# Kernel optimization log

Measured on AMD Instinct MI355X. Metric: run time of the kernel, lower is better.

## Reference

```python
import jax, jax.numpy as jnp
import numpy as np

STRIDES = [8, 16, 32, 64, 128]
CELL_ANCHORS = np.array([
 [[-18.0,-8.0,25.0,15.0],[-23.7183,-11.1191,30.7183,18.1191],[-30.9228,-15.0488,37.9228,22.0488],[-12.0,-12.0,19.0,19.0],[-16.1587,-16.1587,23.1587,23.1587],[-21.3984,-21.3984,28.3984,28.3984],[-8.0,-20.0,15.0,27.0],[-11.1191,-26.2381,18.1191,33.2381],[-15.0488,-34.0976,22.0488,41.0976]],
 [[-38.0,-16.0,53.0,31.0],[-49.9564,-22.2381,64.9564,37.2381],[-65.0204,-30.0976,80.0204,45.0976],[-24.0,-24.0,39.0,39.0],[-32.3175,-32.3175,47.3175,47.3175],[-42.7968,-42.7968,57.7968,57.7968],[-14.0,-36.0,29.0,51.0],[-19.7183,-47.4365,34.7183,62.4365],[-26.9228,-61.8456,41.9228,76.8456]],
 [[-74.0,-28.0,105.0,59.0],[-97.3929,-39.4365,128.3929,70.4365],[-126.8661,-53.8456,157.8661,84.8456],[-48.0,-48.0,79.0,79.0],[-64.6349,-64.6349,95.6349,95.6349],[-85.5937,-85.5937,116.5937,116.5937],[-30.0,-76.0,61.0,107.0],[-41.9564,-99.9127,72.9564,130.9127],[-57.0204,-130.0409,88.0204,161.0409]],
 [[-150.0,-60.0,213.0,123.0],[-197.3056,-83.9127,260.3056,146.9127],[-256.907,-114.0409,319.907,177.0409],[-96.0,-96.0,159.0,159.0],[-129.2699,-129.2699,192.2699,192.2699],[-171.1873,-171.1873,234.1873,234.1873],[-58.0,-148.0,121.0,211.0],[-81.3929,-194.7858,144.3929,257.7858],[-110.8661,-253.7322,173.8661,316.7322]],
 [[-298.0,-116.0,425.0,243.0],[-392.0914,-162.7858,519.0914,289.7858],[-510.6392,-221.7322,637.6392,348.7322],[-192.0,-192.0,319.0,319.0],[-258.5398,-258.5398,385.5398,385.5398],[-342.3747,-342.3747,469.3747,469.3747],[-118.0,-300.0,245.0,427.0],[-165.3056,-394.6113,292.3056,521.6113],[-224.907,-513.814,351.907,640.814]]], dtype=np.float32)
THRESHOLD = 0.05
TOP_N = 1000
NMS_THR = 0.5
DETECTIONS = 100


def conv3x3(x, w, b):
    y = jax.lax.conv_general_dilated(x, w, (1, 1), ((1, 1), (1, 1)),
                                     dimension_numbers=('NCHW', 'OIHW', 'NCHW'))
    return y + b[None, :, None, None]


def run_head(x, ws, bs):
    for w, b in zip(ws[:-1], bs[:-1]):
        x = jax.nn.relu(conv3x3(x, w, b))
    return conv3x3(x, ws[-1], bs[-1])


def delta2box(deltas, anchors, w, h, stride):
    awh = anchors[:, 2:] - anchors[:, :2] + 1.0
    ctr = anchors[:, :2] + 0.5 * awh
    pctr = deltas[:, :2] * awh + ctr
    pwh = jnp.exp(deltas[:, 2:]) * awh
    M = jnp.array([w * stride - 1.0, h * stride - 1.0], dtype=deltas.dtype)
    clamp = lambda t: jnp.clip(t, 0.0, M)
    return jnp.concatenate([clamp(pctr - 0.5 * pwh), clamp(pctr + 0.5 * pwh - 1.0)], axis=1)


def decode_level(cls_map, box_map, stride, anchors):
    # cls_map: (B, A*C, H, W) post-sigmoid; box_map: (B, A*4, H, W)
    B, AC, H, W = cls_map.shape
    A = anchors.shape[0]
    C = AC // A

    def one(cm, bm):
        flat = cm.reshape(-1)                      # (A*C*H*W,)
        scores, idx = jax.lax.top_k(flat, TOP_N)
        cls = (idx // (W * H)) % C
        x = idx % W
        y = (idx // W) % H
        a = idx // (C * H * W)
        deltas = bm.reshape(A, 4, H, W)[a, :, y, x]      # (TOP_N, 4)
        grid = jnp.stack([x, y, x, y], axis=1).astype(flat.dtype) * stride + anchors[a]
        boxes = delta2box(deltas, grid, W, H, stride)
        valid = scores >= THRESHOLD                # emulates threshold filter + zero padding
        return (jnp.where(valid, scores, 0.0),
                jnp.where(valid[:, None], boxes, 0.0),
                jnp.where(valid, cls.astype(flat.dtype), 0.0))

    return jax.vmap(one)(cls_map, box_map)


def nms_all(scores, boxes, classes):
    # per-class greedy NMS, fixed DETECTIONS output slots
    def one(s, b, c):
        order = jnp.argsort(-s)
        s, b, c = s[order], b[order], c[order]
        areas = (b[:, 2] - b[:, 0] + 1.0) * (b[:, 3] - b[:, 1] + 1.0)
        state = (s > 0,
                 jnp.zeros((DETECTIONS,), s.dtype),
                 jnp.zeros((DETECTIONS, 4), s.dtype),
                 jnp.zeros((DETECTIONS,), s.dtype))

        def body(i, st):
            valid, os_, ob_, oc_ = st
            any_v = jnp.any(valid)
            idx = jnp.argmax(valid)                # first remaining box (highest score)
            bi, si, ci, ai = b[idx], s[idx], c[idx], areas[idx]
            xy1 = jnp.maximum(b[:, :2], bi[:2])
            xy2 = jnp.minimum(b[:, 2:], bi[2:])
            inter = jnp.prod(jnp.clip(xy2 - xy1 + 1.0, 0.0, None), axis=1)
            iou = inter / (areas + ai - inter)
            suppress = (s <= si) & (iou > NMS_THR) & (c == ci)
            valid = valid & jnp.where(any_v, ~suppress, True)
            os_ = os_.at[i].set(jnp.where(any_v, si, 0.0))
            ob_ = ob_.at[i].set(jnp.where(any_v, bi, jnp.zeros_like(bi)))
            oc_ = oc_.at[i].set(jnp.where(any_v, ci, 0.0))
            return (valid, os_, ob_, oc_)

        _, os_, ob_, oc_ = jax.lax.fori_loop(0, DETECTIONS, body, state)
        return os_, ob_, oc_

    return jax.vmap(one)(scores, boxes, classes)


def _forward(feats, cls_ws, cls_bs, box_ws, box_bs):
    cls_heads = [jax.nn.sigmoid(run_head(f, cls_ws, cls_bs)) for f in feats]
    box_heads = [run_head(f, box_ws, box_bs) for f in feats]
    parts = [decode_level(ch, bh, STRIDES[i], jnp.asarray(CELL_ANCHORS[i]))
             for i, (ch, bh) in enumerate(zip(cls_heads, box_heads))]
    scores = jnp.concatenate([p[0] for p in parts], axis=1)
    boxes = jnp.concatenate([p[1] for p in parts], axis=1)
    classes = jnp.concatenate([p[2] for p in parts], axis=1)
    return nms_all(scores, boxes, classes)


def setup_inputs() -> dict:
    key = jax.random.key(0)
    ks = jax.random.split(key, 32)
    B = 2
    sizes = [64, 32, 16, 8, 4]
    inp = {}
    for i, s in enumerate(sizes):
        inp['feat%d' % i] = jax.random.normal(ks[i], (B, 256, s, s), jnp.float32)
    cls_out = [256, 256, 256, 256, 720]
    box_out = [256, 256, 256, 256, 36]
    for i in range(5):
        inp['cls_w%d' % i] = jax.random.normal(ks[5 + i], (cls_out[i], 256, 3, 3), jnp.float32) * 0.01
        inp['cls_b%d' % i] = jnp.zeros((cls_out[i],), jnp.float32)
        inp['box_w%d' % i] = jax.random.normal(ks[15 + i], (box_out[i], 256, 3, 3), jnp.float32) * 0.01
        inp['box_b%d' % i] = jnp.zeros((box_out[i],), jnp.float32)
    return inp


def reference(feat0, feat1, feat2, feat3, feat4,
              cls_w0, cls_w1, cls_w2, cls_w3, cls_w4,
              cls_b0, cls_b1, cls_b2, cls_b3, cls_b4,
              box_w0, box_w1, box_w2, box_w3, box_w4,
              box_b0, box_b1, box_b2, box_b3, box_b4):
    feats = [feat0, feat1, feat2, feat3, feat4]
    cls_ws = [cls_w0, cls_w1, cls_w2, cls_w3, cls_w4]
    cls_bs = [cls_b0, cls_b1, cls_b2, cls_b3, cls_b4]
    box_ws = [box_w0, box_w1, box_w2, box_w3, box_w4]
    box_bs = [box_b0, box_b1, box_b2, box_b3, box_b4]
    return _forward(feats, cls_ws, cls_bs, box_ws, box_bs)
```

## Files before the change

### kernel.cpp

```cpp
#include <hip/hip_runtime.h>
#include <math.h>

typedef unsigned long long U64;
#define CCAP 4096

__constant__ float cANCH[180] = {
  -18.0f,-8.0f,25.0f,15.0f, -23.7183f,-11.1191f,30.7183f,18.1191f, -30.9228f,-15.0488f,37.9228f,22.0488f,
  -12.0f,-12.0f,19.0f,19.0f, -16.1587f,-16.1587f,23.1587f,23.1587f, -21.3984f,-21.3984f,28.3984f,28.3984f,
  -8.0f,-20.0f,15.0f,27.0f, -11.1191f,-26.2381f,18.1191f,33.2381f, -15.0488f,-34.0976f,22.0488f,41.0976f,
  -38.0f,-16.0f,53.0f,31.0f, -49.9564f,-22.2381f,64.9564f,37.2381f, -65.0204f,-30.0976f,80.0204f,45.0976f,
  -24.0f,-24.0f,39.0f,39.0f, -32.3175f,-32.3175f,47.3175f,47.3175f, -42.7968f,-42.7968f,57.7968f,57.7968f,
  -14.0f,-36.0f,29.0f,51.0f, -19.7183f,-47.4365f,34.7183f,62.4365f, -26.9228f,-61.8456f,41.9228f,76.8456f,
  -74.0f,-28.0f,105.0f,59.0f, -97.3929f,-39.4365f,128.3929f,70.4365f, -126.8661f,-53.8456f,157.8661f,84.8456f,
  -48.0f,-48.0f,79.0f,79.0f, -64.6349f,-64.6349f,95.6349f,95.6349f, -85.5937f,-85.5937f,116.5937f,116.5937f,
  -30.0f,-76.0f,61.0f,107.0f, -41.9564f,-99.9127f,72.9564f,130.9127f, -57.0204f,-130.0409f,88.0204f,161.0409f,
  -150.0f,-60.0f,213.0f,123.0f, -197.3056f,-83.9127f,260.3056f,146.9127f, -256.907f,-114.0409f,319.907f,177.0409f,
  -96.0f,-96.0f,159.0f,159.0f, -129.2699f,-129.2699f,192.2699f,192.2699f, -171.1873f,-171.1873f,234.1873f,234.1873f,
  -58.0f,-148.0f,121.0f,211.0f, -81.3929f,-194.7858f,144.3929f,257.7858f, -110.8661f,-253.7322f,173.8661f,316.7322f,
  -298.0f,-116.0f,425.0f,243.0f, -392.0914f,-162.7858f,519.0914f,289.7858f, -510.6392f,-221.7322f,637.6392f,348.7322f,
  -192.0f,-192.0f,319.0f,319.0f, -258.5398f,-258.5398f,385.5398f,385.5398f, -342.3747f,-342.3747f,469.3747f,469.3747f,
  -118.0f,-300.0f,245.0f,427.0f, -165.3056f,-394.6113f,292.3056f,521.6113f, -224.907f,-513.814f,351.907f,640.814f
};

__device__ __constant__ int dH[5]      = {64,32,16,8,4};
__device__ __constant__ int dLogW[5]   = {6,5,4,3,2};
__device__ __constant__ int dHW[5]     = {4096,1024,256,64,16};
__device__ __constant__ int dPW[5]     = {66,34,18,10,6};
__device__ __constant__ int dPS[5]     = {4356,1156,324,100,36};
__device__ __constant__ int dPadOff[5] = {0,2230272,2822144,2988032,3039232};
__device__ __constant__ int dCO[5]     = {0,5898240,7372800,7741440,7833600};
__device__ __constant__ int dBO[5]     = {0,294912,368640,387072,391680};
__device__ __constant__ float dStrF[5] = {8.f,16.f,32.f,64.f,128.f};
__device__ __constant__ int dBase[6]   = {0,32,40,42,44,46};
__device__ __constant__ int dNPB[5]    = {16,4,1,1,1};

__global__ void fill_zero4(float4* __restrict__ p, int n4) {
  for (int i = blockIdx.x*blockDim.x + threadIdx.x; i < n4; i += gridDim.x*blockDim.x)
    p[i] = make_float4(0.f,0.f,0.f,0.f);
}

__global__ void pad_one(const float* __restrict__ f, float* __restrict__ P,
                        int n, int logHW, int logW, int W, int PW, int PS) {
  const int HW1 = (1<<logHW) - 1;
  for (int i = blockIdx.x*blockDim.x + threadIdx.x; i < n; i += gridDim.x*blockDim.x) {
    const int bc = i >> logHW;
    const int p  = i & HW1;
    const int y = p >> logW, x = p & (W-1);
    P[(size_t)bc*PS + (y+1)*PW + (x+1)] = f[i];
  }
}

__global__ void transp_w(const float* __restrict__ w, float* __restrict__ wT,
                         int Cout, int OCP) {
  const int n = 9*256*OCP;
  for (int i = blockIdx.x*blockDim.x + threadIdx.x; i < n; i += gridDim.x*blockDim.x) {
    const int oc = i % OCP;
    const int kt = i / OCP;
    const int k  = kt % 256;
    const int t  = kt / 256;
    wT[i] = (oc < Cout) ? w[(size_t)oc*2304 + k*9 + t] : 0.f;
  }
}

__global__ __launch_bounds__(256)
void conv_hidden(const float* __restrict__ IN, float* __restrict__ OUT,
                 const float* __restrict__ wT, const float* __restrict__ bias)
{
  const int bx = blockIdx.x;
  if (bx >= 46) return;
  int l = 0;
  if (bx >= dBase[1]) l = 1;
  if (bx >= dBase[2]) l = 2;
  if (bx >= dBase[3]) l = 3;
  if (bx >= dBase[4]) l = 4;
  const int npb = dNPB[l];
  const int rel = bx - dBase[l];
  const int b = rel / npb, pb = rel % npb;
  const int W = dH[l], logW = dLogW[l], HW = dHW[l], PW = dPW[l], PS = dPS[l];
  const int pix = pb*256 + threadIdx.x;
  if (pix >= HW) return;
  const int y = pix >> logW, x = pix & (W-1);
  const int voff = (y+1)*PW + (x+1);
  const float* __restrict__ inB = IN + (size_t)dPadOff[l] + (size_t)b*256*PS;
  const int oc0 = blockIdx.y * 16;
  float acc[16];
#pragma unroll
  for (int o = 0; o < 16; ++o) acc[o] = 0.f;
#pragma unroll 1
  for (int t = 0; t < 9; ++t) {
    const int dy = t / 3, dx = t - dy * 3;
    const float* __restrict__ ip = inB + (voff + (dy-1)*PW + (dx-1));
    const float* __restrict__ wp = wT + (size_t)t*256*256 + oc0;
#pragma unroll 1
    for (int k0 = 0; k0 < 256; k0 += 16) {
      float v[16];
#pragma unroll
      for (int u = 0; u < 16; ++u) v[u] = ip[(size_t)(k0+u)*PS];
#pragma unroll
      for (int u = 0; u < 16; ++u) {
        const float* __restrict__ w = wp + (size_t)(k0+u)*256;
#pragma unroll
        for (int o = 0; o < 16; ++o) acc[o] = fmaf(w[o], v[u], acc[o]);
      }
    }
  }
  float* __restrict__ op = OUT + (size_t)dPadOff[l] + ((size_t)b*256 + oc0)*PS + voff;
#pragma unroll
  for (int o = 0; o < 16; ++o) {
    const float tv = acc[o] + bias[oc0 + o];
    op[(size_t)o*PS] = fmaxf(tv, 0.f);
  }
}

__global__ __launch_bounds__(256)
void conv_final(const float* __restrict__ IN, float* __restrict__ OUT,
                const float* __restrict__ wT, const float* __restrict__ bias,
                int Cout, int OCL, int isCls)
{
  const int bx = blockIdx.x;
  if (bx >= 46) return;
  int l = 0;
  if (bx >= dBase[1]) l = 1;
  if (bx >= dBase[2]) l = 2;
  if (bx >= dBase[3]) l = 3;
  if (bx >= dBase[4]) l = 4;
  const int npb = dNPB[l];
  const int rel = bx - dBase[l];
  const int b = rel / npb, pb = rel % npb;
  const int W = dH[l], logW = dLogW[l], HW = dHW[l], PW = dPW[l], PS = dPS[l];
  const int pix = pb*256 + threadIdx.x;
  if (pix >= HW) return;
  const int y = pix >> logW, x = pix & (W-1);
  const int voff = (y+1)*PW + (x+1);
  const float* __restrict__ inB = IN + (size_t)dPadOff[l] + (size_t)b*256*PS;
  const int oc0 = blockIdx.y * 16;
  float acc[16];
#pragma unroll
  for (int o = 0; o < 16; ++o) acc[o] = 0.f;
#pragma unroll 1
  for (int t = 0; t < 9; ++t) {
    const int dy = t / 3, dx = t - dy * 3;
    const float* __restrict__ ip = inB + (voff + (dy-1)*PW + (dx-1));
    const float* __restrict__ wp = wT + (size_t)t*256*OCL + oc0;
#pragma unroll 1
    for (int k0 = 0; k0 < 256; k0 += 16) {
      float v[16];
#pragma unroll
      for (int u = 0; u < 16; ++u) v[u] = ip[(size_t)(k0+u)*PS];
#pragma unroll
      for (int u = 0; u < 16; ++u) {
        const float* __restrict__ w = wp + (size_t)(k0+u)*OCL;
#pragma unroll
        for (int o = 0; o < 16; ++o) acc[o] = fmaf(w[o], v[u], acc[o]);
      }
    }
  }
  const int outOff = isCls ? dCO[l] : dBO[l];
#pragma unroll
  for (int o = 0; o < 16; ++o) {
    const int oc = oc0 + o;
    if (oc < Cout) {
      float tv = acc[o] + bias[oc];
      if (isCls) tv = 1.f / (1.f + expf(-tv));
      OUT[(size_t)outOff + ((size_t)b*Cout + oc)*HW + pix] = tv;
    }
  }
}

__global__ void topk_init(unsigned* __restrict__ hist, unsigned* __restrict__ state) {
  for (int i = threadIdx.x; i < 2560; i += blockDim.x) hist[i] = 0u;
  if (threadIdx.x < 10) {
    state[threadIdx.x*4+0] = 0u; state[threadIdx.x*4+1] = 1000u;
    state[threadIdx.x*4+2] = 0u; state[threadIdx.x*4+3] = 0u;
  }
}

__global__ void topk_hist(const float* __restrict__ clsm, unsigned* __restrict__ hist,
                          const unsigned* __restrict__ state, int pass)
{
  __shared__ unsigned lh[256];
  const int id = blockIdx.y, l = id % 5, b = id / 5;
  const int N = 720 * dHW[l];
  const float* __restrict__ sp = clsm + dCO[l] + (size_t)b*720*dHW[l];
  for (int i = threadIdx.x; i < 256; i += blockDim.x) lh[i] = 0u;
  __syncthreads();
  const unsigned prefix = state[id*4];
  for (int i = blockIdx.x*blockDim.x + threadIdx.x; i < N; i += gridDim.x*blockDim.x) {
    const unsigned bits = __float_as_uint(sp[i]);
    unsigned bin; bool ok;
    if (pass == 0)      { bin = bits >> 24;          ok = true; }
    else if (pass == 1) { bin = (bits >> 16) & 0xFF; ok = ((bits >> 24) == prefix); }
    else                { bin = (bits >>  8) & 0xFF; ok = ((bits >> 16) == prefix); }
    if (ok) atomicAdd(&lh[bin], 1u);
  }
  __syncthreads();
  for (int i = threadIdx.x; i < 256; i += blockDim.x)
    if (lh[i]) atomicAdd(&hist[id*256 + i], lh[i]);
}

__global__ void topk_scan(unsigned* __restrict__ hist, unsigned* __restrict__ state) {
  const int id = threadIdx.x;
  if (id < 10) {
    const unsigned k = state[id*4+1];
    unsigned cum = 0; int d = 255;
    for (; d > 0; --d) {
      const unsigned h = hist[id*256 + d];
      if (cum + h >= k) break;
      cum += h;
    }
    state[id*4+0] = (state[id*4+0] << 8) | (unsigned)d;
    state[id*4+1] = k - cum;
  }
  __syncthreads();
  for (int i = threadIdx.x; i < 2560; i += blockDim.x) hist[i] = 0u;
}

__global__ void topk_compact(const float* __restrict__ clsm, unsigned* __restrict__ state,
                             U64* __restrict__ cbuf)
{
  const int id = blockIdx.y, l = id % 5, b = id / 5;
  const int N = 720 * dHW[l];
  const float* __restrict__ sp = clsm + dCO[l] + (size_t)b*720*dHW[l];
  const unsigned p24 = state[id*4];
  for (int i = blockIdx.x*blockDim.x + threadIdx.x; i < N; i += gridDim.x*blockDim.x) {
    const unsigned bits = __float_as_uint(sp[i]);
    if ((bits >> 8) >= p24) {
      const unsigned pos = atomicAdd(&state[id*4+2], 1u);
      if (pos < CCAP)
        cbuf[(size_t)id*CCAP + pos] = ((U64)bits << 32) | (U64)(0xFFFFFFFFu - (unsigned)i);
    }
  }
}

__global__ __launch_bounds__(1024)
void topk_sort_store(const U64* __restrict__ cbuf, const unsigned* __restrict__ state,
                     float* __restrict__ cand_s, float* __restrict__ cand_c,
                     unsigned* __restrict__ sel)
{
  __shared__ U64 sk[CCAP];
  const int id = blockIdx.x, l = id % 5, b = id / 5;
  const int t = threadIdx.x;
  unsigned M = state[id*4+2]; if (M > (unsigned)CCAP) M = CCAP;
  for (int i = t; i < CCAP; i += 1024) sk[i] = (i < (int)M) ? cbuf[(size_t)id*CCAP + i] : 0ull;
  __syncthreads();
  for (int k = 2; k <= CCAP; k <<= 1)
    for (int j = k >> 1; j > 0; j >>= 1) {
      for (int u = t; u < CCAP/2; u += 1024) {
        const int i1 = ((u & ~(j-1)) << 1) | (u & (j-1));
        const int i2 = i1 + j;
        const bool asc = ((i1 & k) == 0);
        const U64 a = sk[i1], c = sk[i2];
        if ((a < c) == asc) { sk[i1] = c; sk[i2] = a; }
      }
      __syncthreads();
    }
  const int HW = dHW[l];
  for (int j = t; j < 1000; j += 1024) {
    float sc_ = 0.f, cf = 0.f; unsigned sidx = 0xFFFFFFFFu;
    if (j < (int)M) {
      const U64 key = sk[j];
      const float s = __uint_as_float((unsigned)(key >> 32));
      const unsigned idx = 0xFFFFFFFFu - (unsigned)key;
      if (s >= 0.05f) {
        const int ch = (int)(idx / (unsigned)HW);
        const int cls = ch % 80;
        sc_ = s; cf = (float)cls; sidx = idx;
      }
    }
    const int slot = b*5000 + l*1000 + j;
    cand_s[slot] = sc_; cand_c[slot] = cf; sel[slot] = sidx;
  }
}

__global__ __launch_bounds__(1024)
void box_decode(const float* __restrict__ boxm, const float* __restrict__ cand_s,
                const unsigned* __restrict__ sel, float4* __restrict__ cand_b)
{
  const int id = blockIdx.x, l = id % 5, b = id / 5;
  const int HW = dHW[l], W = dH[l], logW = dLogW[l];
  const float stride = dStrF[l];
  const int j = threadIdx.x;
  if (j >= 1000) return;
  const int slot = b*5000 + l*1000 + j;
  float4 bx = make_float4(0.f,0.f,0.f,0.f);
  if (cand_s[slot] > 0.f) {
    const unsigned idx = sel[slot];
    const int pix = (int)(idx & (unsigned)(HW-1));
    const int ch  = (int)(idx >> (2*logW));
    const int a   = ch / 80;
    const int xx = pix & (W-1), yy = pix >> logW;
    const float* __restrict__ bm = boxm + dBO[l] + (size_t)b*36*HW;
    const float d0 = bm[(size_t)(a*4+0)*HW + pix];
    const float d1 = bm[(size_t)(a*4+1)*HW + pix];
    const float d2 = bm[(size_t)(a*4+2)*HW + pix];
    const float d3 = bm[(size_t)(a*4+3)*HW + pix];
    const float* A = &cANCH[l*36 + a*4];
    const float g0 = (float)xx * stride + A[0];
    const float g1 = (float)yy * stride + A[1];
    const float g2 = (float)xx * stride + A[2];
    const float g3 = (float)yy * stride + A[3];
    const float awx = g2 - g0 + 1.f, awy = g3 - g1 + 1.f;
    const float cx = g0 + 0.5f*awx, cy = g1 + 0.5f*awy;
    const float pcx = d0*awx + cx, pcy = d1*awy + cy;
    const float pwx = expf(d2)*awx, pwy = expf(d3)*awy;
    const float Mx = (float)W*stride - 1.f, My = (float)W*stride - 1.f;
    const float x1 = fminf(fmaxf(pcx - 0.5f*pwx, 0.f), Mx);
    const float y1 = fminf(fmaxf(pcy - 0.5f*pwy, 0.f), My);
    const float x2 = fminf(fmaxf(pcx + 0.5f*pwx - 1.f, 0.f), Mx);
    const float y2 = fminf(fmaxf(pcy + 0.5f*pwy - 1.f, 0.f), My);
    bx = make_float4(x1, y1, x2, y2);
  }
  cand_b[slot] = bx;
}

__global__ __launch_bounds__(1024)
void nms_sort(const float* __restrict__ cs, const float4* __restrict__ cb, const float* __restrict__ cc,
              float* __restrict__ ss, float4* __restrict__ sb, float* __restrict__ sc)
{
  extern __shared__ U64 sk[];
  const int b = blockIdx.x;
  const int t = threadIdx.x;
  for (int i = t; i < 8192; i += 1024) {
    U64 key = 0ull;
    if (i < 5000) {
      const unsigned bits = __float_as_uint(cs[b*5000 + i]);
      key = ((U64)bits << 32) | (U64)(0xFFFFFFFFu - (unsigned)i);
    }
    sk[i] = key;
  }
  __syncthreads();
  for (int k = 2; k <= 8192; k <<= 1)
    for (int j = k >> 1; j > 0; j >>= 1) {
      for (int u = t; u < 4096; u += 1024) {
        const int i1 = ((u & ~(j-1)) << 1) | (u & (j-1));
        const int i2 = i1 + j;
        const bool asc = ((i1 & k) == 0);
        const U64 a = sk[i1], c = sk[i2];
        if ((a < c) == asc) { sk[i1] = c; sk[i2] = a; }
      }
      __syncthreads();
    }
  for (int i = t; i < 5000; i += 1024) {
    const unsigned pos = 0xFFFFFFFFu - (unsigned)sk[i];
    ss[b*5008 + i] = cs[b*5000 + pos];
    sb[b*5008 + i] = cb[b*5000 + pos];
    sc[b*5008 + i] = cc[b*5000 + pos];
  }
}

__global__ __launch_bounds__(1024)
void nms_greedy(const float* __restrict__ ss, const float4* __restrict__ sb, const float* __restrict__ sc,
                float* __restrict__ outp)
{
  const int b = blockIdx.x;
  const int t = threadIdx.x;
  __shared__ int red[16];
  __shared__ int selSh;
  __shared__ float bc[8];

  const float* SS = ss + (size_t)b*5008;
  const float4* SB = sb + (size_t)b*5008;
  const float* SC = sc + (size_t)b*5008;

  float s[5], c[5], ar[5]; float4 bx[5]; bool val[5];
#pragma unroll
  for (int k = 0; k < 5; ++k) {
    const int j = t + k*1024;
    if (j < 5000) {
      s[k] = SS[j]; c[k] = SC[j]; bx[k] = SB[j];
      val[k] = (s[k] > 0.f);
      ar[k] = (bx[k].z - bx[k].x + 1.f) * (bx[k].w - bx[k].y + 1.f);
    } else {
      s[k] = 0.f; c[k] = 0.f; bx[k] = make_float4(0.f,0.f,0.f,0.f);
      val[k] = false; ar[k] = 1.f;
    }
  }

  for (int i = 0; i < 100; ++i) {
    int loc = 0x7FFFFFFF;
#pragma unroll
    for (int k = 0; k < 5; ++k) if (val[k]) { const int j = t + k*1024; loc = (j < loc) ? j : loc; }
    for (int off = 32; off > 0; off >>= 1) { const int o = __shfl_down(loc, off); loc = (o < loc) ? o : loc; }
    if ((t & 63) == 0) red[t >> 6] = loc;
    __syncthreads();
    if (t < 64) {
      int v = (t < 16) ? red[t] : 0x7FFFFFFF;
      for (int off = 8; off > 0; off >>= 1) { const int o = __shfl_down(v, off); v = (o < v) ? o : v; }
      if (t == 0) selSh = v;
    }
    __syncthreads();
    const int sel_ = selSh;
    if (sel_ == 0x7FFFFFFF) {
      if (t == 0) {
        outp[b*100 + i] = 0.f;
        outp[200 + (b*100 + i)*4 + 0] = 0.f;
        outp[200 + (b*100 + i)*4 + 1] = 0.f;
        outp[200 + (b*100 + i)*4 + 2] = 0.f;
        outp[200 + (b*100 + i)*4 + 3] = 0.f;
        outp[1000 + b*100 + i] = 0.f;
      }
    } else {
      if (t == (sel_ & 1023)) {
        const int k = sel_ >> 10;
        bc[0] = s[k]; bc[1] = c[k];
        bc[2] = bx[k].x; bc[3] = bx[k].y; bc[4] = bx[k].z; bc[5] = bx[k].w;
        bc[6] = ar[k];
        outp[b*100 + i] = s[k];
        outp[200 + (b*100 + i)*4 + 0] = bx[k].x;
        outp[200 + (b*100 + i)*4 + 1] = bx[k].y;
        outp[200 + (b*100 + i)*4 + 2] = bx[k].z;
        outp[200 + (b*100 + i)*4 + 3] = bx[k].w;
        outp[1000 + b*100 + i] = c[k];
      }
      __syncthreads();
      const float si = bc[0], ci = bc[1], ai = bc[6];
      const float bix = bc[2], biy = bc[3], biz = bc[4], biw = bc[5];
#pragma unroll
      for (int k = 0; k < 5; ++k) {
        if (!val[k]) continue;
        const float xx1 = fmaxf(bx[k].x, bix), yy1 = fmaxf(bx[k].y, biy);
        const float xx2 = fminf(bx[k].z, biz), yy2 = fminf(bx[k].w, biw);
        const float iw = fmaxf(xx2 - xx1 + 1.f, 0.f), ih = fmaxf(yy2 - yy1 + 1.f, 0.f);
        const float inter = iw * ih;
        const float iou = inter / (ar[k] + ai - inter);
        if (s[k] <= si && iou > 0.5f && c[k] == ci) val[k] = false;
      }
    }
    __syncthreads();
  }
}

extern "C" void kernel_launch(void* const* d_in, const int* in_sizes, int n_in,
                              void* d_out, int out_size, void* d_ws, size_t ws_size,
                              hipStream_t stream)
{
  (void)in_sizes; (void)n_in; (void)out_size; (void)ws_size;
  const float* feat[5]; const float* cwp[5]; const float* cbp[5]; const float* bwp[5]; const float* bbp[5];
  for (int i = 0; i < 5; ++i) feat[i] = (const float*)d_in[i];
  for (int i = 0; i < 5; ++i) {
    cwp[i] = (const float*)d_in[5 + 4*i + 0];
    cbp[i] = (const float*)d_in[5 + 4*i + 1];
    bwp[i] = (const float*)d_in[5 + 4*i + 2];
    bbp[i] = (const float*)d_in[5 + 4*i + 3];
  }

  float* ws = (float*)d_ws;
  const size_t BUFSZ = 3057664;
  float* P     = ws;
  float* A     = ws + BUFSZ;
  float* Bb    = ws + 2*BUFSZ;
  float* clsm  = ws + 3*BUFSZ;
  float* boxm  = clsm + 7856640;
  float* wT    = boxm + 392832;
  float* cand_s = wT + 1769472;
  float* cand_b = cand_s + 10000;
  float* cand_c = cand_b + 40000;
  float* srt_s  = cand_c + 10000;
  float* srt_b  = srt_s + 10016;
  float* srt_c  = srt_b + 40064;
  unsigned* sel   = (unsigned*)(srt_c + 10016);
  unsigned* hist  = (unsigned*)(srt_c + 20016);
  unsigned* state = (unsigned*)(srt_c + 22576);
  U64*      cbuf  = (U64*)(srt_c + 22616);

  const int hHW[5]    = {4096,1024,256,64,16};
  const int hLogHW[5] = {12,10,8,6,4};
  const int hLogW[5]  = {6,5,4,3,2};
  const int hW[5]     = {64,32,16,8,4};
  const int hPW[5]    = {66,34,18,10,6};
  const int hPS[5]    = {4356,1156,324,100,36};
  const int hPadOff[5]= {0,2230272,2822144,2988032,3039232};

  fill_zero4<<<2048, 256, 0, stream>>>((float4*)P, (int)(3*BUFSZ/4));

  for (int l = 0; l < 5; ++l) {
    const int n = 2*256*hHW[l];
    int g = (n + 255)/256; if (g > 2048) g = 2048;
    pad_one<<<g, 256, 0, stream>>>(feat[l], P + hPadOff[l], n, hLogHW[l], hLogW[l],
                                   hW[l], hPW[l], hPS[l]);
  }

  auto runHidden = [&](const float* w, const float* bias, const float* src, float* dst) {
    transp_w<<<2304, 256, 0, stream>>>(w, wT, 256, 256);
    conv_hidden<<<dim3(48, 16), dim3(256), 0, stream>>>(src, dst, wT, bias);
  };

  runHidden(cwp[0], cbp[0], P,  A);
  runHidden(cwp[1], cbp[1], A,  Bb);
  runHidden(cwp[2], cbp[2], Bb, A);
  runHidden(cwp[3], cbp[3], A,  Bb);
  transp_w<<<6480, 256, 0, stream>>>(cwp[4], wT, 720, 720);
  conv_final<<<dim3(48, 45), dim3(256), 0, stream>>>(Bb, clsm, wT, cbp[4], 720, 720, 1);

  topk_init<<<1, 1024, 0, stream>>>(hist, state);
  for (int pass = 0; pass < 3; ++pass) {
    topk_hist<<<dim3(128, 10), dim3(256), 0, stream>>>(clsm, hist, state, pass);
    topk_scan<<<1, 256, 0, stream>>>(hist, state);
  }
  topk_compact<<<dim3(128, 10), dim3(256), 0, stream>>>(clsm, state, cbuf);
  topk_sort_store<<<10, 1024, 0, stream>>>(cbuf, state, cand_s, cand_c, sel);

  runHidden(bwp[0], bbp[0], P,  A);
  runHidden(bwp[1], bbp[1], A,  Bb);
  runHidden(bwp[2], bbp[2], Bb, A);
  runHidden(bwp[3], bbp[3], A,  Bb);
  transp_w<<<432, 256, 0, stream>>>(bwp[4], wT, 36, 48);
  conv_final<<<dim3(48, 3), dim3(256), 0, stream>>>(Bb, boxm, wT, bbp[4], 36, 48, 0);

  box_decode<<<10, 1024, 0, stream>>>(boxm, cand_s, sel, (float4*)cand_b);

  nms_sort<<<dim3(2), dim3(1024), 8192*sizeof(U64), stream>>>(
      cand_s, (const float4*)cand_b, cand_c, srt_s, (float4*)srt_b, srt_c);
  nms_greedy<<<dim3(2), dim3(1024), 0, stream>>>(
      srt_s, (const float4*)srt_b, srt_c, (float*)d_out);
}
```

Measured before the change: 3.239 ms.

## Pack activations in channel-quad interleaved layout for float4 loads in convs

Switches the padded activation buffers from planar NCHW to a layout where each group of four channels is interleaved per pixel. The pad kernel, hidden conv and final conv all read and write this layout, so each thread issues one 16-byte load per four channels instead of four scalar loads. The aim is fewer memory instructions and wider transactions in the direct convolution inner loop. Every pass over the activations now moves strided float4 data across lanes, which may change coalescing.

```diff
diff --git a/kernel.cpp b/kernel.cpp
--- a/kernel.cpp
+++ b/kernel.cpp
@@ -39,14 +39,16 @@
     p[i] = make_float4(0.f,0.f,0.f,0.f);
 }
 
-__global__ void pad_one(const float* __restrict__ f, float* __restrict__ P,
-                        int n, int logHW, int logW, int W, int PW, int PS) {
+__global__ void pad_one_p4(const float* __restrict__ f, float* __restrict__ P,
+                           int n, int logHW, int logW, int W, int PW, int PS) {
   const int HW1 = (1<<logHW) - 1;
   for (int i = blockIdx.x*blockDim.x + threadIdx.x; i < n; i += gridDim.x*blockDim.x) {
     const int bc = i >> logHW;
     const int p  = i & HW1;
+    const int b = bc >> 8, c = bc & 255;
     const int y = p >> logW, x = p & (W-1);
-    P[(size_t)bc*PS + (y+1)*PW + (x+1)] = f[i];
+    const int vpix = (y+1)*PW + (x+1);
+    P[(((size_t)(b*64 + (c>>2)))*PS + vpix)*4 + (c&3)] = f[i];
   }
 }
 
@@ -62,10 +64,23 @@
   }
 }
 
+#define QUAD(KB, Q)                                                     \
+  {                                                                     \
+    const float* __restrict__ w0 = wp + (size_t)((KB)+0)*OCL;           \
+    const float* __restrict__ w1 = wp + (size_t)((KB)+1)*OCL;           \
+    const float* __restrict__ w2 = wp + (size_t)((KB)+2)*OCL;           \
+    const float* __restrict__ w3 = wp + (size_t)((KB)+3)*OCL;           \
+    _Pragma("unroll") for (int o=0;o<16;++o) acc[o]=fmaf(w0[o],(Q).x,acc[o]); \
+    _Pragma("unroll") for (int o=0;o<16;++o) acc[o]=fmaf(w1[o],(Q).y,acc[o]); \
+    _Pragma("unroll") for (int o=0;o<16;++o) acc[o]=fmaf(w2[o],(Q).z,acc[o]); \
+    _Pragma("unroll") for (int o=0;o<16;++o) acc[o]=fmaf(w3[o],(Q).w,acc[o]); \
+  }
+
 __global__ __launch_bounds__(256)
 void conv_hidden(const float* __restrict__ IN, float* __restrict__ OUT,
                  const float* __restrict__ wT, const float* __restrict__ bias)
 {
+  const int OCL = 256;
   const int bx = blockIdx.x;
   if (bx >= 46) return;
   int l = 0;
@@ -81,7 +96,8 @@
   if (pix >= HW) return;
   const int y = pix >> logW, x = pix & (W-1);
   const int voff = (y+1)*PW + (x+1);
-  const float* __restrict__ inB = IN + (size_t)dPadOff[l] + (size_t)b*256*PS;
+  const float4* __restrict__ P4 = (const float4*)(IN + dPadOff[l]);
+  const float4* __restrict__ inB = P4 + (size_t)b*64*PS + voff;
   const int oc0 = blockIdx.y * 16;
   float acc[16];
 #pragma unroll
@@ -89,26 +105,31 @@
 #pragma unroll 1
   for (int t = 0; t < 9; ++t) {
     const int dy = t / 3, dx = t - dy * 3;
-    const float* __restrict__ ip = inB + (voff + (dy-1)*PW + (dx-1));
-    const float* __restrict__ wp = wT + (size_t)t*256*256 + oc0;
+    const float4* __restrict__ ip = inB + ((dy-1)*PW + (dx-1));
+    const float* __restrict__ wp = wT + (size_t)t*256*OCL + oc0;
 #pragma unroll 1
     for (int k0 = 0; k0 < 256; k0 += 16) {
-      float v[16];
-#pragma unroll
-      for (int u = 0; u < 16; ++u) v[u] = ip[(size_t)(k0+u)*PS];
-#pragma unroll
-      for (int u = 0; u < 16; ++u) {
-        const float* __restrict__ w = wp + (size_t)(k0+u)*256;
-#pragma unroll
-        for (int o = 0; o < 16; ++o) acc[o] = fmaf(w[o], v[u], acc[o]);
-      }
-    }
-  }
-  float* __restrict__ op = OUT + (size_t)dPadOff[l] + ((size_t)b*256 + oc0)*PS + voff;
-#pragma unroll
-  for (int o = 0; o < 16; ++o) {
-    const float tv = acc[o] + bias[oc0 + o];
-    op[(size_t)o*PS] = fmaxf(tv, 0.f);
+      const int kq = k0 >> 2;
+      const float4 q0 = ip[(size_t)(kq+0)*PS];
+      const float4 q1 = ip[(size_t)(kq+1)*PS];
+      const float4 q2 = ip[(size_t)(kq+2)*PS];
+      const float4 q3 = ip[(size_t)(kq+3)*PS];
+      QUAD(k0+ 0, q0);
+      QUAD(k0+ 4, q1);
+      QUAD(k0+ 8, q2);
+      QUAD(k0+12, q3);
+    }
+  }
+  float4* __restrict__ O4 = (float4*)(OUT + dPadOff[l]);
+  float4* __restrict__ op = O4 + ((size_t)b*64 + (oc0 >> 2))*PS + voff;
+#pragma unroll
+  for (int j = 0; j < 4; ++j) {
+    const float4 sv = make_float4(
+      fmaxf(acc[4*j+0] + bias[oc0+4*j+0], 0.f),
+      fmaxf(acc[4*j+1] + bias[oc0+4*j+1], 0.f),
+      fmaxf(acc[4*j+2] + bias[oc0+4*j+2], 0.f),
+      fmaxf(acc[4*j+3] + bias[oc0+4*j+3], 0.f));
+    op[(size_t)j*PS] = sv;
   }
 }
 
@@ -132,7 +153,8 @@
   if (pix >= HW) return;
   const int y = pix >> logW, x = pix & (W-1);
   const int voff = (y+1)*PW + (x+1);
-  const float* __restrict__ inB = IN + (size_t)dPadOff[l] + (size_t)b*256*PS;
+  const float4* __restrict__ P4 = (const float4*)(IN + dPadOff[l]);
+  const float4* __restrict__ inB = P4 + (size_t)b*64*PS + voff;
   const int oc0 = blockIdx.y * 16;
   float acc[16];
 #pragma unroll
@@ -140,19 +162,19 @@
 #pragma unroll 1
   for (int t = 0; t < 9; ++t) {
     const int dy = t / 3, dx = t - dy * 3;
-    const float* __restrict__ ip = inB + (voff + (dy-1)*PW + (dx-1));
+    const float4* __restrict__ ip = inB + ((dy-1)*PW + (dx-1));
     const float* __restrict__ wp = wT + (size_t)t*256*OCL + oc0;
 #pragma unroll 1
     for (int k0 = 0; k0 < 256; k0 += 16) {
-      float v[16];
-#pragma unroll
-      for (int u = 0; u < 16; ++u) v[u] = ip[(size_t)(k0+u)*PS];
-#pragma unroll
-      for (int u = 0; u < 16; ++u) {
-        const float* __restrict__ w = wp + (size_t)(k0+u)*OCL;
-#pragma unroll
-        for (int o = 0; o < 16; ++o) acc[o] = fmaf(w[o], v[u], acc[o]);
-      }
+      const int kq = k0 >> 2;
+      const float4 q0 = ip[(size_t)(kq+0)*PS];
+      const float4 q1 = ip[(size_t)(kq+1)*PS];
+      const float4 q2 = ip[(size_t)(kq+2)*PS];
+      const float4 q3 = ip[(size_t)(kq+3)*PS];
+      QUAD(k0+ 0, q0);
+      QUAD(k0+ 4, q1);
+      QUAD(k0+ 8, q2);
+      QUAD(k0+12, q3);
     }
   }
   const int outOff = isCls ? dCO[l] : dBO[l];
@@ -476,8 +498,8 @@
   for (int l = 0; l < 5; ++l) {
     const int n = 2*256*hHW[l];
     int g = (n + 255)/256; if (g > 2048) g = 2048;
-    pad_one<<<g, 256, 0, stream>>>(feat[l], P + hPadOff[l], n, hLogHW[l], hLogW[l],
-                                   hW[l], hPW[l], hPS[l]);
+    pad_one_p4<<<g, 256, 0, stream>>>(feat[l], P + hPadOff[l], n, hLogHW[l], hLogW[l],
+                                      hW[l], hPW[l], hPS[l]);
   }
 
   auto runHidden = [&](const float* w, const float* bias, const float* src, float* dst) {
```

Measured after the change: 3.169 ms. 1.02x faster.
